# Kernel tuning notes

Hardware: AMD Instinct MI355X
Metric: run time of the kernel (lower is better)

## Reference

```python
import jax, jax.numpy as jnp
import numpy as np

HIDDEN = 512
HEADS = 8
HEAD_DIM = HIDDEN // HEADS


def setup_inputs() -> dict:
    key = jax.random.key(0)
    ks = jax.random.split(key, 7)
    B, C, H, W = 8, HIDDEN, 32, 32
    scale = 1.0 / np.sqrt(C)
    inputs = jax.random.normal(ks[0], (B, C, H, W), dtype=jnp.float32)
    # 1x1 conv == per-pixel linear; store weights as [C_in, C_out]
    wq = jax.random.normal(ks[1], (C, HIDDEN), dtype=jnp.float32) * scale
    wk = jax.random.normal(ks[2], (C, HIDDEN), dtype=jnp.float32) * scale
    wv = jax.random.normal(ks[3], (C, HIDDEN), dtype=jnp.float32) * scale
    bq = jax.random.normal(ks[4], (HIDDEN,), dtype=jnp.float32) * 0.01
    bk = jax.random.normal(ks[5], (HIDDEN,), dtype=jnp.float32) * 0.01
    bv = jax.random.normal(ks[6], (HIDDEN,), dtype=jnp.float32) * 0.01
    return {"inputs": inputs, "wq": wq, "bq": bq, "wk": wk, "bk": bk, "wv": wv, "bv": bv}


def _proj_heads(x, w, b):
    # x: [B,C,H,W] -> tokens [B,heads,N,head_dim], matching transpose_for_scores
    B, C, H, W = x.shape
    t = jnp.einsum('bchw,cd->bhwd', x, w) + b          # [B,H,W,HIDDEN]
    t = t.reshape(B, H * W, HEADS, HEAD_DIM)
    return t.transpose(0, 2, 1, 3)                      # [B,heads,N,hd]


def reference(inputs, wq, bq, wk, bk, wv, bv):
    B, C, H, W = inputs.shape
    q = _proj_heads(inputs, wq, bq)
    k = _proj_heads(inputs, wk, bk)
    v = _proj_heads(inputs, wv, bv)
    # NOTE: original module applies NO 1/sqrt(d) scaling
    scores = jnp.einsum('bhnd,bhmd->bhnm', q, k)        # [B,heads,N,N]
    probs = jax.nn.softmax(scores, axis=-1)
    ctx = jnp.einsum('bhnm,bhmd->bhnd', probs, v)       # [B,heads,N,hd]
    # [B,heads,N,hd] -> [B,N,heads*hd] -> [B,H,W,C] -> [B,C,H,W]
    out = ctx.transpose(0, 2, 1, 3).reshape(B, H, W, HEADS * HEAD_DIM)
    return out.transpose(0, 3, 1, 2)
```

## Files before the change

### kernel.cpp

```cpp
#include <hip/hip_runtime.h>
#include <cmath>

#define B_     8
#define C_     512
#define N_     1024
#define HEADS_ 8
#define HD_    64
#define INST_  64

typedef short v8s  __attribute__((ext_vector_type(8)));
typedef float v16f __attribute__((ext_vector_type(16)));
typedef unsigned short ushort_t;
typedef unsigned int   uint_t;

__device__ inline unsigned short f2bf(float x) {
    unsigned u = __builtin_bit_cast(unsigned, x);
    unsigned r = u + 0x7fffu + ((u >> 16) & 1u);
    return (unsigned short)(r >> 16);
}
__device__ inline float bf2f(unsigned short h) {
    unsigned u = ((unsigned)h) << 16;
    return __builtin_bit_cast(float, u);
}

__global__ __launch_bounds__(256) void prep_kernel(
    const float* __restrict__ x,
    const float* __restrict__ wq, const float* __restrict__ wk,
    const float* __restrict__ wv,
    uint_t* __restrict__ wth, uint_t* __restrict__ wtl,
    uint_t* __restrict__ xth, uint_t* __restrict__ xtl)
{
    __shared__ uint_t LH[64 * 32];
    __shared__ uint_t LL[64 * 32];
    const int z = blockIdx.z;
    const float* src;
    int srcStride;
    size_t outRow0;
    uint_t *oh, *ol;
    if (z < 3) {
        if (blockIdx.x >= 8) return;
        src = (z == 0) ? wq : (z == 1) ? wk : wv;
        srcStride = 512;
        outRow0 = (size_t)z * 512 + blockIdx.x * 64;
        oh = wth; ol = wtl;
    } else {
        int b = z - 3;
        src = x + (size_t)b * C_ * N_;
        srcStride = 1024;
        outRow0 = (size_t)b * 1024 + blockIdx.x * 64;
        oh = xth; ol = xtl;
    }
    const int d0 = blockIdx.x * 64;
    const int c0 = blockIdx.y * 64;
    const int t  = threadIdx.x;

    #pragma unroll
    for (int rep = 0; rep < 2; ++rep) {
        int idx = rep * 256 + t;
        int cp  = idx >> 4;
        int dq  = idx & 15;
        float4 fa = *(const float4*)&src[(size_t)(c0 + 2 * cp) * srcStride + d0 + dq * 4];
        float4 fb = *(const float4*)&src[(size_t)(c0 + 2 * cp + 1) * srcStride + d0 + dq * 4];
        float aa[4] = {fa.x, fa.y, fa.z, fa.w};
        float bb[4] = {fb.x, fb.y, fb.z, fb.w};
        #pragma unroll
        for (int j = 0; j < 4; ++j) {
            int d_l = dq * 4 + j;
            unsigned short ha = f2bf(aa[j]), hb = f2bf(bb[j]);
            unsigned short la = f2bf(aa[j] - bf2f(ha));
            unsigned short lb = f2bf(bb[j] - bf2f(hb));
            LH[d_l * 32 + (cp ^ (d_l & 31))] = (uint_t)ha | ((uint_t)hb << 16);
            LL[d_l * 32 + (cp ^ (d_l & 31))] = (uint_t)la | ((uint_t)lb << 16);
        }
    }
    __syncthreads();

    const int d_l = t >> 2;
    const int wq4 = (t & 3) * 8;
    uint_t vh[8], vl[8];
    #pragma unroll
    for (int i = 0; i < 8; ++i) {
        vh[i] = LH[d_l * 32 + ((wq4 + i) ^ (d_l & 31))];
        vl[i] = LL[d_l * 32 + ((wq4 + i) ^ (d_l & 31))];
    }
    size_t base = (outRow0 + d_l) * 256 + c0 / 2 + wq4;
    *(uint4*)&oh[base]     = *(uint4*)&vh[0];
    *(uint4*)&oh[base + 4] = *(uint4*)&vh[4];
    *(uint4*)&ol[base]     = *(uint4*)&vl[0];
    *(uint4*)&ol[base + 4] = *(uint4*)&vl[4];
}

__global__ __launch_bounds__(256) void proj_kernel(
    const ushort_t* __restrict__ xth, const ushort_t* __restrict__ xtl,
    const ushort_t* __restrict__ wth, const ushort_t* __restrict__ wtl,
    const float* __restrict__ bq, const float* __restrict__ bk,
    const float* __restrict__ bv,
    ushort_t* __restrict__ qh, ushort_t* __restrict__ ql,
    ushort_t* __restrict__ kh, ushort_t* __restrict__ kl,
    ushort_t* __restrict__ vt)
{
    __shared__ uint_t POOL[8192];
    ushort_t* As = (ushort_t*)POOL;
    ushort_t* Bs = (ushort_t*)(POOL + 4096);

    const int tok0  = blockIdx.x * 128;
    const int b     = tok0 >> 10;
    const int ntb   = tok0 & 1023;
    const int by    = blockIdx.y;
    const int which = by >> 2;
    const int nloc0 = (by & 3) * 128;

    const int t   = threadIdx.x;
    const int w   = t >> 6;
    const int l   = t & 63;
    const int l31 = l & 31;
    const int h5  = l >> 5;
    const int wm  = w & 1;
    const int wn  = w >> 1;

    const int g   = t & 7;
    const int r0  = t >> 3;
    const int swz = g ^ (r0 & 7);
    const bool act = (which < 2) || (g < 4);

    const ushort_t* baseA = ((g < 4) ? xth : xtl)
        + (size_t)(tok0 + r0) * 512 + (g & 3) * 8;
    const ushort_t* baseB = ((g < 4) ? wth : wtl)
        + (size_t)(which * 512 + nloc0 + r0) * 512 + (g & 3) * 8;

    v8s pfa[4], pfb[4];

    auto load_tile = [&](int k0) {
        #pragma unroll
        for (int rep = 0; rep < 4; ++rep)
            if (act) {
                pfa[rep] = *(const v8s*)(baseA + rep * 16384 + k0);
                pfb[rep] = *(const v8s*)(baseB + rep * 16384 + k0);
            }
    };
    auto store_tile = [&]() {
        #pragma unroll
        for (int rep = 0; rep < 4; ++rep)
            if (act) {
                int so = ((rep * 32 + r0) * 8 + swz) * 8;
                *(v8s*)&As[so] = pfa[rep];
                *(v8s*)&Bs[so] = pfb[rep];
            }
    };

    v16f acc[2][2] = {{{}, {}}, {{}, {}}};

    load_tile(0);
    store_tile();
    __syncthreads();

    for (int step = 0; step < 16; ++step) {
        if (step < 15) load_tile((step + 1) * 32);

        #pragma unroll
        for (int kc = 0; kc < 2; ++kc) {
            v8s ahf[2], alf[2], bhf[2], blf[2];
            #pragma unroll
            for (int ms = 0; ms < 2; ++ms) {
                int rm = wm * 64 + ms * 32 + l31;
                ahf[ms] = *(v8s*)&As[(rm * 8 + ((kc * 2 + h5) ^ (rm & 7))) * 8];
                if (which < 2)
                    alf[ms] = *(v8s*)&As[(rm * 8 + ((4 + kc * 2 + h5) ^ (rm & 7))) * 8];
            }
            #pragma unroll
            for (int ns = 0; ns < 2; ++ns) {
                int rn = wn * 64 + ns * 32 + l31;
                bhf[ns] = *(v8s*)&Bs[(rn * 8 + ((kc * 2 + h5) ^ (rn & 7))) * 8];
                if (which < 2)
                    blf[ns] = *(v8s*)&Bs[(rn * 8 + ((4 + kc * 2 + h5) ^ (rn & 7))) * 8];
            }
            #pragma unroll
            for (int ms = 0; ms < 2; ++ms)
                #pragma unroll
                for (int ns = 0; ns < 2; ++ns) {
                    acc[ms][ns] = __builtin_amdgcn_mfma_f32_32x32x16_bf16(
                        ahf[ms], bhf[ns], acc[ms][ns], 0, 0, 0);
                    if (which < 2) {
                        acc[ms][ns] = __builtin_amdgcn_mfma_f32_32x32x16_bf16(
                            alf[ms], bhf[ns], acc[ms][ns], 0, 0, 0);
                        acc[ms][ns] = __builtin_amdgcn_mfma_f32_32x32x16_bf16(
                            ahf[ms], blf[ns], acc[ms][ns], 0, 0, 0);
                    }
                }
        }

        __syncthreads();
        if (step < 15) {
            store_tile();
            __syncthreads();
        }
    }

    if (which < 2) {
        ushort_t* oh = (which == 0) ? qh : kh;
        ushort_t* ol = (which == 0) ? ql : kl;
        const float* bias = (which == 0) ? bq : bk;
        #pragma unroll
        for (int ns = 0; ns < 2; ++ns) {
            int d_local = nloc0 + wn * 64 + ns * 32 + l31;
            float bvv  = bias[d_local];
            int head   = d_local >> 6;
            int hd     = d_local & 63;
            size_t pb  = (size_t)(b * HEADS_ + head) * 65536 + hd;
            #pragma unroll
            for (int ms = 0; ms < 2; ++ms)
                #pragma unroll
                for (int r = 0; r < 16; ++r) {
                    int n = ntb + wm * 64 + ms * 32 + (r & 3) + 8 * (r >> 2) + 4 * h5;
                    float val = acc[ms][ns][r] + bvv;
                    unsigned short hbits = f2bf(val);
                    oh[pb + (size_t)n * 64] = hbits;
                    ol[pb + (size_t)n * 64] = f2bf(val - bf2f(hbits));
                }
        }
    } else {
        float bvv[2];
        #pragma unroll
        for (int ns = 0; ns < 2; ++ns)
            bvv[ns] = bv[nloc0 + wn * 64 + ns * 32 + l31];
        __syncthreads();
        uint_t* TW = POOL + w * 2048;
        #pragma unroll
        for (int ms = 0; ms < 2; ++ms)
            #pragma unroll
            for (int ns = 0; ns < 2; ++ns)
                #pragma unroll
                for (int r = 0; r < 16; ++r) {
                    int tok_l = ms * 32 + (r & 3) + 8 * (r >> 2) + 4 * h5;
                    int hd_l  = ns * 32 + l31;
                    unsigned short hbits = f2bf(acc[ms][ns][r] + bvv[ns]);
                    ((ushort_t*)TW)[(hd_l * 32 + ((tok_l >> 1) ^ (hd_l & 31))) * 2
                                    + (tok_l & 1)] = hbits;
                }
        __syncthreads();
        const int head = (nloc0 + wn * 64) >> 6;
        uint_t* vtu = (uint_t*)vt;
        size_t base = (size_t)(b * HEADS_ + head) * 32768 + (size_t)l * 512
                    + (ntb + wm * 64) / 2;
        #pragma unroll
        for (int c = 0; c < 8; ++c) {
            uint_t wd[4];
            #pragma unroll
            for (int kk = 0; kk < 4; ++kk) {
                int ws = c * 4 + kk;
                int w3 = ws & 7;
                int sw = (ws & ~7) | (w3 & 1) | (((w3 >> 1) & 1) << 2)
                                  | (((w3 >> 2) & 1) << 1);
                wd[kk] = TW[l * 32 + (sw ^ (l & 31))];
            }
            *(uint4*)&vtu[base + c * 4] = *(uint4*)&wd[0];
        }
    }
}

__global__ __launch_bounds__(256) void attn_kernel(
    const ushort_t* __restrict__ qh, const ushort_t* __restrict__ ql,
    const ushort_t* __restrict__ kh, const ushort_t* __restrict__ kl,
    const ushort_t* __restrict__ vt, float* __restrict__ out)
{
    __shared__ ushort_t KH[64 * 64];
    __shared__ ushort_t KL[64 * 64];
    __shared__ ushort_t VT[64 * 64];
    __shared__ float    RS[128];

    const int inst  = blockIdx.x;
    const int chunk = blockIdx.y;
    const int t     = threadIdx.x;
    const int w     = t >> 6;
    const int l     = t & 63;
    const int l31   = l & 31;
    const int h5    = l >> 5;

    const ushort_t* Qh = qh + (size_t)inst * 65536;
    const ushort_t* Ql = ql + (size_t)inst * 65536;
    const ushort_t* Kh = kh + (size_t)inst * 65536;
    const ushort_t* Kl = kl + (size_t)inst * 65536;
    const ushort_t* Vt = vt + (size_t)inst * 65536;

    const int qbase = chunk * 128 + w * 32;

    v8s aqh[4], aql[4];
    #pragma unroll
    for (int ks = 0; ks < 4; ++ks) {
        size_t off = (size_t)(qbase + l31) * 64 + ks * 16 + h5 * 8;
        aqh[ks] = *(const v8s*)&Qh[off];
        aql[ks] = *(const v8s*)&Ql[off];
    }

    const int g   = t & 7;
    const int r0  = t >> 3;
    const int swz = g ^ (r0 & 7);
    const ushort_t* baseKh = Kh + (size_t)r0 * 64 + g * 8;
    const ushort_t* baseKl = Kl + (size_t)r0 * 64 + g * 8;
    const ushort_t* baseV  = Vt + (size_t)r0 * 1024 + g * 8;

    v8s pk[2], pl[2], pv[2];
    auto load_tile = [&](int kt) {
        #pragma unroll
        for (int rep = 0; rep < 2; ++rep) {
            pk[rep] = *(const v8s*)(baseKh + (size_t)kt * 4096 + rep * 2048);
            pl[rep] = *(const v8s*)(baseKl + (size_t)kt * 4096 + rep * 2048);
            pv[rep] = *(const v8s*)(baseV + (size_t)rep * 32768 + kt * 64);
        }
    };
    auto store_tile = [&]() {
        #pragma unroll
        for (int rep = 0; rep < 2; ++rep) {
            int so = ((rep * 32 + r0) * 8 + swz) * 8;
            *(v8s*)&KH[so] = pk[rep];
            *(v8s*)&KL[so] = pl[rep];
            *(v8s*)&VT[so] = pv[rep];
        }
    };

    v16f O0 = {}, O1 = {};
    float rsumv = 0.f;

    load_tile(0);
    store_tile();
    __syncthreads();

    for (int kt = 0; kt < 16; ++kt) {
        if (kt < 15) load_tile(kt + 1);

        #pragma unroll
        for (int t2 = 0; t2 < 2; ++t2) {
            v16f s = {};
            int kvrow = t2 * 32 + l31;
            #pragma unroll
            for (int ks = 0; ks < 4; ++ks) {
                int so = (kvrow * 8 + ((ks * 2 + h5) ^ (kvrow & 7))) * 8;
                v8s khf = *(v8s*)&KH[so];
                v8s klf = *(v8s*)&KL[so];
                s = __builtin_amdgcn_mfma_f32_32x32x16_bf16(khf, aqh[ks], s, 0, 0, 0);
                s = __builtin_amdgcn_mfma_f32_32x32x16_bf16(khf, aql[ks], s, 0, 0, 0);
                s = __builtin_amdgcn_mfma_f32_32x32x16_bf16(klf, aqh[ks], s, 0, 0, 0);
            }
            v8s p0, p1;
            #pragma unroll
            for (int j = 0; j < 8; ++j) {
                float e0 = __expf(s[j] - 64.0f);
                float e1 = __expf(s[8 + j] - 64.0f);
                rsumv += e0 + e1;
                p0[j] = (short)f2bf(e0);
                p1[j] = (short)f2bf(e1);
            }
            #pragma unroll
            for (int hh = 0; hh < 2; ++hh) {
                int rv = hh * 32 + l31;
                int g0 = (4 * t2 + h5)     ^ (rv & 7);
                int g1 = (4 * t2 + 2 + h5) ^ (rv & 7);
                v8s bv0 = *(v8s*)&VT[(rv * 8 + g0) * 8];
                v8s bv1 = *(v8s*)&VT[(rv * 8 + g1) * 8];
                if (hh == 0) {
                    O0 = __builtin_amdgcn_mfma_f32_32x32x16_bf16(p0, bv0, O0, 0, 0, 0);
                    O0 = __builtin_amdgcn_mfma_f32_32x32x16_bf16(p1, bv1, O0, 0, 0, 0);
                } else {
                    O1 = __builtin_amdgcn_mfma_f32_32x32x16_bf16(p0, bv0, O1, 0, 0, 0);
                    O1 = __builtin_amdgcn_mfma_f32_32x32x16_bf16(p1, bv1, O1, 0, 0, 0);
                }
            }
        }

        __syncthreads();
        if (kt < 15) {
            store_tile();
            __syncthreads();
        }
    }

    float tot = rsumv + __shfl_xor(rsumv, 32, 64);
    if (h5 == 0) RS[w * 32 + l31] = 1.0f / tot;
    __syncthreads();
    float invr[16];
    #pragma unroll
    for (int r = 0; r < 16; ++r)
        invr[r] = RS[w * 32 + (r & 3) + 8 * (r >> 2) + 4 * h5];

    const int b    = inst >> 3;
    const int head = inst & 7;
    float* ob = out + (size_t)b * C_ * N_;
    #pragma unroll
    for (int hh = 0; hh < 2; ++hh) {
        const v16f& O = hh ? O1 : O0;
        int c = head * 64 + hh * 32 + l31;
        #pragma unroll
        for (int qd = 0; qd < 4; ++qd) {
            int n = qbase + 8 * qd + 4 * h5;
            float4 o4;
            o4.x = O[qd * 4 + 0] * invr[qd * 4 + 0];
            o4.y = O[qd * 4 + 1] * invr[qd * 4 + 1];
            o4.z = O[qd * 4 + 2] * invr[qd * 4 + 2];
            o4.w = O[qd * 4 + 3] * invr[qd * 4 + 3];
            *(float4*)&ob[(size_t)c * N_ + n] = o4;
        }
    }
}

extern "C" void kernel_launch(void* const* d_in, const int* in_sizes, int n_in,
                              void* d_out, int out_size, void* d_ws, size_t ws_size,
                              hipStream_t stream) {
    const float* x  = (const float*)d_in[0];
    const float* wq = (const float*)d_in[1];
    const float* bq = (const float*)d_in[2];
    const float* wk = (const float*)d_in[3];
    const float* bk = (const float*)d_in[4];
    const float* wv = (const float*)d_in[5];
    const float* bv = (const float*)d_in[6];
    float* out = (float*)d_out;

    char* ws = (char*)d_ws;
    ushort_t* wth = (ushort_t*)(ws);
    ushort_t* wtl = (ushort_t*)(ws + 1572864);
    ushort_t* xth = (ushort_t*)(ws + 3145728);
    ushort_t* xtl = (ushort_t*)(ws + 11534336);
    ushort_t* qh  = (ushort_t*)(ws + 19922944);
    ushort_t* ql  = (ushort_t*)(ws + 28311552);
    ushort_t* kh  = (ushort_t*)(ws + 36700160);
    ushort_t* kl  = (ushort_t*)(ws + 45088768);
    ushort_t* vt  = (ushort_t*)(ws + 53477376);

    prep_kernel<<<dim3(16, 8, 11), 256, 0, stream>>>(
        x, wq, wk, wv, (uint_t*)wth, (uint_t*)wtl, (uint_t*)xth, (uint_t*)xtl);
    proj_kernel<<<dim3(64, 12), 256, 0, stream>>>(xth, xtl, wth, wtl,
                                                  bq, bk, bv, qh, ql, kh, kl, vt);
    attn_kernel<<<dim3(64, 8), 256, 0, stream>>>(qh, ql, kh, kl, vt, out);
}
```

Measured before the change: 167.6 us.

## Double-buffer LDS tiles in projection and attention kernels, split prep kernel

Converts the projection and attention main loops to double-buffered shared memory so the next tile is stored into the alternate buffer. This removes one barrier per iteration and issues global loads two steps ahead. It also splits the combined weight and input prep kernel into two kernels, which drops the early-exit blocks. Packed bf16 conversion via the HIP intrinsic replaces scalar conversions in the softmax and V-transpose paths. The cost is doubled LDS use, which may lower occupancy, plus one extra kernel launch.

```diff
diff --git a/kernel.cpp b/kernel.cpp
--- a/kernel.cpp
+++ b/kernel.cpp
@@ -1,4 +1,5 @@
 #include <hip/hip_runtime.h>
+#include <hip/hip_bf16.h>
 #include <cmath>
 
 #define B_     8
@@ -22,34 +23,22 @@
     unsigned u = ((unsigned)h) << 16;
     return __builtin_bit_cast(float, u);
 }
-
-__global__ __launch_bounds__(256) void prep_kernel(
-    const float* __restrict__ x,
+__device__ inline uint_t pkbf(float a, float b) {
+    __hip_bfloat162 p = __float22bfloat162_rn(make_float2(a, b));
+    uint_t r;
+    __builtin_memcpy(&r, &p, 4);
+    return r;
+}
+
+__global__ __launch_bounds__(256) void prep_w_kernel(
     const float* __restrict__ wq, const float* __restrict__ wk,
     const float* __restrict__ wv,
-    uint_t* __restrict__ wth, uint_t* __restrict__ wtl,
-    uint_t* __restrict__ xth, uint_t* __restrict__ xtl)
+    uint_t* __restrict__ wth, uint_t* __restrict__ wtl)
 {
     __shared__ uint_t LH[64 * 32];
     __shared__ uint_t LL[64 * 32];
-    const int z = blockIdx.z;
-    const float* src;
-    int srcStride;
-    size_t outRow0;
-    uint_t *oh, *ol;
-    if (z < 3) {
-        if (blockIdx.x >= 8) return;
-        src = (z == 0) ? wq : (z == 1) ? wk : wv;
-        srcStride = 512;
-        outRow0 = (size_t)z * 512 + blockIdx.x * 64;
-        oh = wth; ol = wtl;
-    } else {
-        int b = z - 3;
-        src = x + (size_t)b * C_ * N_;
-        srcStride = 1024;
-        outRow0 = (size_t)b * 1024 + blockIdx.x * 64;
-        oh = xth; ol = xtl;
-    }
+    const int which = blockIdx.z;
+    const float* __restrict__ src = (which == 0) ? wq : (which == 1) ? wk : wv;
     const int d0 = blockIdx.x * 64;
     const int c0 = blockIdx.y * 64;
     const int t  = threadIdx.x;
@@ -59,8 +48,8 @@
         int idx = rep * 256 + t;
         int cp  = idx >> 4;
         int dq  = idx & 15;
-        float4 fa = *(const float4*)&src[(size_t)(c0 + 2 * cp) * srcStride + d0 + dq * 4];
-        float4 fb = *(const float4*)&src[(size_t)(c0 + 2 * cp + 1) * srcStride + d0 + dq * 4];
+        float4 fa = *(const float4*)&src[(size_t)(c0 + 2 * cp) * 512 + d0 + dq * 4];
+        float4 fb = *(const float4*)&src[(size_t)(c0 + 2 * cp + 1) * 512 + d0 + dq * 4];
         float aa[4] = {fa.x, fa.y, fa.z, fa.w};
         float bb[4] = {fb.x, fb.y, fb.z, fb.w};
         #pragma unroll
@@ -83,11 +72,59 @@
         vh[i] = LH[d_l * 32 + ((wq4 + i) ^ (d_l & 31))];
         vl[i] = LL[d_l * 32 + ((wq4 + i) ^ (d_l & 31))];
     }
-    size_t base = (outRow0 + d_l) * 256 + c0 / 2 + wq4;
-    *(uint4*)&oh[base]     = *(uint4*)&vh[0];
-    *(uint4*)&oh[base + 4] = *(uint4*)&vh[4];
-    *(uint4*)&ol[base]     = *(uint4*)&vl[0];
-    *(uint4*)&ol[base + 4] = *(uint4*)&vl[4];
+    size_t base = ((size_t)which * 512 + d0 + d_l) * 256 + c0 / 2 + wq4;
+    *(uint4*)&wth[base]     = *(uint4*)&vh[0];
+    *(uint4*)&wth[base + 4] = *(uint4*)&vh[4];
+    *(uint4*)&wtl[base]     = *(uint4*)&vl[0];
+    *(uint4*)&wtl[base + 4] = *(uint4*)&vl[4];
+}
+
+__global__ __launch_bounds__(256) void prep_x_kernel(
+    const float* __restrict__ x,
+    uint_t* __restrict__ xth, uint_t* __restrict__ xtl)
+{
+    __shared__ uint_t LH[64 * 32];
+    __shared__ uint_t LL[64 * 32];
+    const int b = blockIdx.z;
+    const float* __restrict__ src = x + (size_t)b * C_ * N_;
+    const int d0 = blockIdx.x * 64;
+    const int c0 = blockIdx.y * 64;
+    const int t  = threadIdx.x;
+
+    #pragma unroll
+    for (int rep = 0; rep < 2; ++rep) {
+        int idx = rep * 256 + t;
+        int cp  = idx >> 4;
+        int dq  = idx & 15;
+        float4 fa = *(const float4*)&src[(size_t)(c0 + 2 * cp) * 1024 + d0 + dq * 4];
+        float4 fb = *(const float4*)&src[(size_t)(c0 + 2 * cp + 1) * 1024 + d0 + dq * 4];
+        float aa[4] = {fa.x, fa.y, fa.z, fa.w};
+        float bb[4] = {fb.x, fb.y, fb.z, fb.w};
+        #pragma unroll
+        for (int j = 0; j < 4; ++j) {
+            int d_l = dq * 4 + j;
+            unsigned short ha = f2bf(aa[j]), hb = f2bf(bb[j]);
+            unsigned short la = f2bf(aa[j] - bf2f(ha));
+            unsigned short lb = f2bf(bb[j] - bf2f(hb));
+            LH[d_l * 32 + (cp ^ (d_l & 31))] = (uint_t)ha | ((uint_t)hb << 16);
+            LL[d_l * 32 + (cp ^ (d_l & 31))] = (uint_t)la | ((uint_t)lb << 16);
+        }
+    }
+    __syncthreads();
+
+    const int d_l = t >> 2;
+    const int wq4 = (t & 3) * 8;
+    uint_t vh[8], vl[8];
+    #pragma unroll
+    for (int i = 0; i < 8; ++i) {
+        vh[i] = LH[d_l * 32 + ((wq4 + i) ^ (d_l & 31))];
+        vl[i] = LL[d_l * 32 + ((wq4 + i) ^ (d_l & 31))];
+    }
+    size_t base = ((size_t)b * 1024 + d0 + d_l) * 256 + c0 / 2 + wq4;
+    *(uint4*)&xth[base]     = *(uint4*)&vh[0];
+    *(uint4*)&xth[base + 4] = *(uint4*)&vh[4];
+    *(uint4*)&xtl[base]     = *(uint4*)&vl[0];
+    *(uint4*)&xtl[base + 4] = *(uint4*)&vl[4];
 }
 
 __global__ __launch_bounds__(256) void proj_kernel(
@@ -99,9 +136,7 @@
     ushort_t* __restrict__ kh, ushort_t* __restrict__ kl,
     ushort_t* __restrict__ vt)
 {
-    __shared__ uint_t POOL[8192];
-    ushort_t* As = (ushort_t*)POOL;
-    ushort_t* Bs = (ushort_t*)(POOL + 4096);
+    __shared__ ushort_t POOL[32768];
 
     const int tok0  = blockIdx.x * 128;
     const int b     = tok0 >> 10;
@@ -138,7 +173,9 @@
                 pfb[rep] = *(const v8s*)(baseB + rep * 16384 + k0);
             }
     };
-    auto store_tile = [&]() {
+    auto store_tile = [&](int buf) {
+        ushort_t* As = POOL + buf * 16384;
+        ushort_t* Bs = As + 8192;
         #pragma unroll
         for (int rep = 0; rep < 4; ++rep)
             if (act) {
@@ -151,11 +188,13 @@
     v16f acc[2][2] = {{{}, {}}, {{}, {}}};
 
     load_tile(0);
-    store_tile();
+    store_tile(0);
+    load_tile(32);
     __syncthreads();
 
     for (int step = 0; step < 16; ++step) {
-        if (step < 15) load_tile((step + 1) * 32);
+        const ushort_t* As = POOL + (step & 1) * 16384;
+        const ushort_t* Bs = As + 8192;
 
         #pragma unroll
         for (int kc = 0; kc < 2; ++kc) {
@@ -163,16 +202,16 @@
             #pragma unroll
             for (int ms = 0; ms < 2; ++ms) {
                 int rm = wm * 64 + ms * 32 + l31;
-                ahf[ms] = *(v8s*)&As[(rm * 8 + ((kc * 2 + h5) ^ (rm & 7))) * 8];
+                ahf[ms] = *(const v8s*)&As[(rm * 8 + ((kc * 2 + h5) ^ (rm & 7))) * 8];
                 if (which < 2)
-                    alf[ms] = *(v8s*)&As[(rm * 8 + ((4 + kc * 2 + h5) ^ (rm & 7))) * 8];
+                    alf[ms] = *(const v8s*)&As[(rm * 8 + ((4 + kc * 2 + h5) ^ (rm & 7))) * 8];
             }
             #pragma unroll
             for (int ns = 0; ns < 2; ++ns) {
                 int rn = wn * 64 + ns * 32 + l31;
-                bhf[ns] = *(v8s*)&Bs[(rn * 8 + ((kc * 2 + h5) ^ (rn & 7))) * 8];
+                bhf[ns] = *(const v8s*)&Bs[(rn * 8 + ((kc * 2 + h5) ^ (rn & 7))) * 8];
                 if (which < 2)
-                    blf[ns] = *(v8s*)&Bs[(rn * 8 + ((4 + kc * 2 + h5) ^ (rn & 7))) * 8];
+                    blf[ns] = *(const v8s*)&Bs[(rn * 8 + ((4 + kc * 2 + h5) ^ (rn & 7))) * 8];
             }
             #pragma unroll
             for (int ms = 0; ms < 2; ++ms)
@@ -189,10 +228,10 @@
                 }
         }
 
-        __syncthreads();
         if (step < 15) {
-            store_tile();
+            store_tile((step + 1) & 1);
             __syncthreads();
+            if (step < 14) load_tile((step + 2) * 32);
         }
     }
 
@@ -224,18 +263,17 @@
         for (int ns = 0; ns < 2; ++ns)
             bvv[ns] = bv[nloc0 + wn * 64 + ns * 32 + l31];
         __syncthreads();
-        uint_t* TW = POOL + w * 2048;
+        uint_t* TW = (uint_t*)POOL + w * 2048;
         #pragma unroll
         for (int ms = 0; ms < 2; ++ms)
             #pragma unroll
             for (int ns = 0; ns < 2; ++ns)
                 #pragma unroll
-                for (int r = 0; r < 16; ++r) {
+                for (int r = 0; r < 16; r += 2) {
                     int tok_l = ms * 32 + (r & 3) + 8 * (r >> 2) + 4 * h5;
                     int hd_l  = ns * 32 + l31;
-                    unsigned short hbits = f2bf(acc[ms][ns][r] + bvv[ns]);
-                    ((ushort_t*)TW)[(hd_l * 32 + ((tok_l >> 1) ^ (hd_l & 31))) * 2
-                                    + (tok_l & 1)] = hbits;
+                    TW[hd_l * 32 + ((tok_l >> 1) ^ (hd_l & 31))] =
+                        pkbf(acc[ms][ns][r] + bvv[ns], acc[ms][ns][r + 1] + bvv[ns]);
                 }
         __syncthreads();
         const int head = (nloc0 + wn * 64) >> 6;
@@ -247,10 +285,10 @@
             uint_t wd[4];
             #pragma unroll
             for (int kk = 0; kk < 4; ++kk) {
-                int ws = c * 4 + kk;
-                int w3 = ws & 7;
-                int sw = (ws & ~7) | (w3 & 1) | (((w3 >> 1) & 1) << 2)
-                                  | (((w3 >> 2) & 1) << 1);
+                int wsx = c * 4 + kk;
+                int w3 = wsx & 7;
+                int sw = (wsx & ~7) | (w3 & 1) | (((w3 >> 1) & 1) << 2)
+                                   | (((w3 >> 2) & 1) << 1);
                 wd[kk] = TW[l * 32 + (sw ^ (l & 31))];
             }
             *(uint4*)&vtu[base + c * 4] = *(uint4*)&wd[0];
@@ -263,9 +301,7 @@
     const ushort_t* __restrict__ kh, const ushort_t* __restrict__ kl,
     const ushort_t* __restrict__ vt, float* __restrict__ out)
 {
-    __shared__ ushort_t KH[64 * 64];
-    __shared__ ushort_t KL[64 * 64];
-    __shared__ ushort_t VT[64 * 64];
+    __shared__ ushort_t POOL[24576];
     __shared__ float    RS[128];
 
     const int inst  = blockIdx.x;
@@ -308,7 +344,10 @@
             pv[rep] = *(const v8s*)(baseV + (size_t)rep * 32768 + kt * 64);
         }
     };
-    auto store_tile = [&]() {
+    auto store_tile = [&](int buf) {
+        ushort_t* KH = POOL + buf * 12288;
+        ushort_t* KL = KH + 4096;
+        ushort_t* VT = KL + 4096;
         #pragma unroll
         for (int rep = 0; rep < 2; ++rep) {
             int so = ((rep * 32 + r0) * 8 + swz) * 8;
@@ -322,11 +361,14 @@
     float rsumv = 0.f;
 
     load_tile(0);
-    store_tile();
+    store_tile(0);
+    load_tile(1);
     __syncthreads();
 
     for (int kt = 0; kt < 16; ++kt) {
-        if (kt < 15) load_tile(kt + 1);
+        const ushort_t* KH = POOL + (kt & 1) * 12288;
+        const ushort_t* KL = KH + 4096;
+        const ushort_t* VT = KL + 4096;
 
         #pragma unroll
         for (int t2 = 0; t2 < 2; ++t2) {
@@ -335,28 +377,34 @@
             #pragma unroll
             for (int ks = 0; ks < 4; ++ks) {
                 int so = (kvrow * 8 + ((ks * 2 + h5) ^ (kvrow & 7))) * 8;
-                v8s khf = *(v8s*)&KH[so];
-                v8s klf = *(v8s*)&KL[so];
+                v8s khf = *(const v8s*)&KH[so];
+                v8s klf = *(const v8s*)&KL[so];
                 s = __builtin_amdgcn_mfma_f32_32x32x16_bf16(khf, aqh[ks], s, 0, 0, 0);
                 s = __builtin_amdgcn_mfma_f32_32x32x16_bf16(khf, aql[ks], s, 0, 0, 0);
                 s = __builtin_amdgcn_mfma_f32_32x32x16_bf16(klf, aqh[ks], s, 0, 0, 0);
             }
-            v8s p0, p1;
+            float e0[8], e1[8];
             #pragma unroll
             for (int j = 0; j < 8; ++j) {
-                float e0 = __expf(s[j] - 64.0f);
-                float e1 = __expf(s[8 + j] - 64.0f);
-                rsumv += e0 + e1;
-                p0[j] = (short)f2bf(e0);
-                p1[j] = (short)f2bf(e1);
-            }
+                e0[j] = __expf(s[j] - 64.0f);
+                e1[j] = __expf(s[8 + j] - 64.0f);
+                rsumv += e0[j] + e1[j];
+            }
+            uint4 u0, u1;
+            u0.x = pkbf(e0[0], e0[1]); u0.y = pkbf(e0[2], e0[3]);
+            u0.z = pkbf(e0[4], e0[5]); u0.w = pkbf(e0[6], e0[7]);
+            u1.x = pkbf(e1[0], e1[1]); u1.y = pkbf(e1[2], e1[3]);
+            u1.z = pkbf(e1[4], e1[5]); u1.w = pkbf(e1[6], e1[7]);
+            v8s p0 = __builtin_bit_cast(v8s, u0);
+            v8s p1 = __builtin_bit_cast(v8s, u1);
+
             #pragma unroll
             for (int hh = 0; hh < 2; ++hh) {
                 int rv = hh * 32 + l31;
                 int g0 = (4 * t2 + h5)     ^ (rv & 7);
                 int g1 = (4 * t2 + 2 + h5) ^ (rv & 7);
-                v8s bv0 = *(v8s*)&VT[(rv * 8 + g0) * 8];
-                v8s bv1 = *(v8s*)&VT[(rv * 8 + g1) * 8];
+                v8s bv0 = *(const v8s*)&VT[(rv * 8 + g0) * 8];
+                v8s bv1 = *(const v8s*)&VT[(rv * 8 + g1) * 8];
                 if (hh == 0) {
                     O0 = __builtin_amdgcn_mfma_f32_32x32x16_bf16(p0, bv0, O0, 0, 0, 0);
                     O0 = __builtin_amdgcn_mfma_f32_32x32x16_bf16(p1, bv1, O0, 0, 0, 0);
@@ -367,10 +415,10 @@
             }
         }
 
-        __syncthreads();
         if (kt < 15) {
-            store_tile();
+            store_tile((kt + 1) & 1);
             __syncthreads();
+            if (kt < 14) load_tile(kt + 2);
         }
     }
 
@@ -425,8 +473,9 @@
     ushort_t* kl  = (ushort_t*)(ws + 45088768);
     ushort_t* vt  = (ushort_t*)(ws + 53477376);
 
-    prep_kernel<<<dim3(16, 8, 11), 256, 0, stream>>>(
-        x, wq, wk, wv, (uint_t*)wth, (uint_t*)wtl, (uint_t*)xth, (uint_t*)xtl);
+    prep_w_kernel<<<dim3(8, 8, 3), 256, 0, stream>>>(wq, wk, wv,
+                                                     (uint_t*)wth, (uint_t*)wtl);
+    prep_x_kernel<<<dim3(16, 8, 8), 256, 0, stream>>>(x, (uint_t*)xth, (uint_t*)xtl);
     proj_kernel<<<dim3(64, 12), 256, 0, stream>>>(xth, xtl, wth, wtl,
                                                   bq, bk, bv, qh, ql, kh, kl, vt);
     attn_kernel<<<dim3(64, 8), 256, 0, stream>>>(qh, ql, kh, kl, vt, out);
```

After: 179.1 us. 1.07x slower.

## Replace split-bf16 emulation with single fp16 MFMA for projections and QK scores

Applied to the files above, without the earlier changes.

Drops the hi/lo bf16 split (three MFMAs per product) in both the projection GEMM and the QK^T score computation and uses a single fp16 MFMA instead. x, W, Q and K are stored as fp16, which halves workspace traffic and LDS footprint and removes two thirds of the MFMAs in those stages. Softmax probabilities and V are now packed to bf16 with a paired conversion intrinsic. This trades accuracy for speed: the unscaled scores are sensitive to reduced mantissa, and fp16 range could overflow for large values.

```diff
diff --git a/kernel.cpp b/kernel.cpp
--- a/kernel.cpp
+++ b/kernel.cpp
@@ -1,4 +1,5 @@
 #include <hip/hip_runtime.h>
+#include <hip/hip_bf16.h>
 #include <cmath>
 
 #define B_     8
@@ -8,47 +9,45 @@
 #define HD_    64
 #define INST_  64
 
-typedef short v8s  __attribute__((ext_vector_type(8)));
-typedef float v16f __attribute__((ext_vector_type(16)));
+typedef short     v8s __attribute__((ext_vector_type(8)));
+typedef _Float16  v8h __attribute__((ext_vector_type(8)));
+typedef float    v16f __attribute__((ext_vector_type(16)));
 typedef unsigned short ushort_t;
 typedef unsigned int   uint_t;
 
-__device__ inline unsigned short f2bf(float x) {
-    unsigned u = __builtin_bit_cast(unsigned, x);
-    unsigned r = u + 0x7fffu + ((u >> 16) & 1u);
-    return (unsigned short)(r >> 16);
-}
-__device__ inline float bf2f(unsigned short h) {
-    unsigned u = ((unsigned)h) << 16;
-    return __builtin_bit_cast(float, u);
+__device__ inline ushort_t f2h(float x) {
+    _Float16 h = (_Float16)x;
+    ushort_t r; __builtin_memcpy(&r, &h, 2); return r;
+}
+__device__ inline uint_t pkbf(float a, float b) {
+    __hip_bfloat162 p = __float22bfloat162_rn(make_float2(a, b));
+    uint_t r; __builtin_memcpy(&r, &p, 4); return r;
 }
 
 __global__ __launch_bounds__(256) void prep_kernel(
     const float* __restrict__ x,
     const float* __restrict__ wq, const float* __restrict__ wk,
     const float* __restrict__ wv,
-    uint_t* __restrict__ wth, uint_t* __restrict__ wtl,
-    uint_t* __restrict__ xth, uint_t* __restrict__ xtl)
+    uint_t* __restrict__ wt, uint_t* __restrict__ xt)
 {
     __shared__ uint_t LH[64 * 32];
-    __shared__ uint_t LL[64 * 32];
     const int z = blockIdx.z;
     const float* src;
     int srcStride;
     size_t outRow0;
-    uint_t *oh, *ol;
+    uint_t* oh;
     if (z < 3) {
         if (blockIdx.x >= 8) return;
         src = (z == 0) ? wq : (z == 1) ? wk : wv;
         srcStride = 512;
         outRow0 = (size_t)z * 512 + blockIdx.x * 64;
-        oh = wth; ol = wtl;
+        oh = wt;
     } else {
         int b = z - 3;
         src = x + (size_t)b * C_ * N_;
         srcStride = 1024;
         outRow0 = (size_t)b * 1024 + blockIdx.x * 64;
-        oh = xth; ol = xtl;
+        oh = xt;
     }
     const int d0 = blockIdx.x * 64;
     const int c0 = blockIdx.y * 64;
@@ -66,42 +65,33 @@
         #pragma unroll
         for (int j = 0; j < 4; ++j) {
             int d_l = dq * 4 + j;
-            unsigned short ha = f2bf(aa[j]), hb = f2bf(bb[j]);
-            unsigned short la = f2bf(aa[j] - bf2f(ha));
-            unsigned short lb = f2bf(bb[j] - bf2f(hb));
-            LH[d_l * 32 + (cp ^ (d_l & 31))] = (uint_t)ha | ((uint_t)hb << 16);
-            LL[d_l * 32 + (cp ^ (d_l & 31))] = (uint_t)la | ((uint_t)lb << 16);
+            LH[d_l * 32 + (cp ^ (d_l & 31))] =
+                (uint_t)f2h(aa[j]) | ((uint_t)f2h(bb[j]) << 16);
         }
     }
     __syncthreads();
 
     const int d_l = t >> 2;
     const int wq4 = (t & 3) * 8;
-    uint_t vh[8], vl[8];
-    #pragma unroll
-    for (int i = 0; i < 8; ++i) {
+    uint_t vh[8];
+    #pragma unroll
+    for (int i = 0; i < 8; ++i)
         vh[i] = LH[d_l * 32 + ((wq4 + i) ^ (d_l & 31))];
-        vl[i] = LL[d_l * 32 + ((wq4 + i) ^ (d_l & 31))];
-    }
     size_t base = (outRow0 + d_l) * 256 + c0 / 2 + wq4;
     *(uint4*)&oh[base]     = *(uint4*)&vh[0];
     *(uint4*)&oh[base + 4] = *(uint4*)&vh[4];
-    *(uint4*)&ol[base]     = *(uint4*)&vl[0];
-    *(uint4*)&ol[base + 4] = *(uint4*)&vl[4];
 }
 
 __global__ __launch_bounds__(256) void proj_kernel(
-    const ushort_t* __restrict__ xth, const ushort_t* __restrict__ xtl,
-    const ushort_t* __restrict__ wth, const ushort_t* __restrict__ wtl,
+    const _Float16* __restrict__ xt, const _Float16* __restrict__ wt,
     const float* __restrict__ bq, const float* __restrict__ bk,
     const float* __restrict__ bv,
-    ushort_t* __restrict__ qh, ushort_t* __restrict__ ql,
-    ushort_t* __restrict__ kh, ushort_t* __restrict__ kl,
+    ushort_t* __restrict__ qf, ushort_t* __restrict__ kf,
     ushort_t* __restrict__ vt)
 {
-    __shared__ uint_t POOL[8192];
-    ushort_t* As = (ushort_t*)POOL;
-    ushort_t* Bs = (ushort_t*)(POOL + 4096);
+    __shared__ _Float16 POOL[16384];
+    _Float16* As = POOL;
+    _Float16* Bs = POOL + 4096;
 
     const int tok0  = blockIdx.x * 128;
     const int b     = tok0 >> 10;
@@ -118,34 +108,28 @@
     const int wm  = w & 1;
     const int wn  = w >> 1;
 
-    const int g   = t & 7;
-    const int r0  = t >> 3;
-    const int swz = g ^ (r0 & 7);
-    const bool act = (which < 2) || (g < 4);
-
-    const ushort_t* baseA = ((g < 4) ? xth : xtl)
-        + (size_t)(tok0 + r0) * 512 + (g & 3) * 8;
-    const ushort_t* baseB = ((g < 4) ? wth : wtl)
-        + (size_t)(which * 512 + nloc0 + r0) * 512 + (g & 3) * 8;
-
-    v8s pfa[4], pfb[4];
-
+    const int g   = t & 3;
+    const int r0  = t >> 2;
+    const int swz = g ^ (r0 & 3);
+
+    const _Float16* baseA = xt + (size_t)(tok0 + r0) * 512 + g * 8;
+    const _Float16* baseB = wt + (size_t)(which * 512 + nloc0 + r0) * 512 + g * 8;
+
+    v8h pfa[2], pfb[2];
     auto load_tile = [&](int k0) {
         #pragma unroll
-        for (int rep = 0; rep < 4; ++rep)
-            if (act) {
-                pfa[rep] = *(const v8s*)(baseA + rep * 16384 + k0);
-                pfb[rep] = *(const v8s*)(baseB + rep * 16384 + k0);
-            }
+        for (int rep = 0; rep < 2; ++rep) {
+            pfa[rep] = *(const v8h*)(baseA + rep * 32768 + k0);
+            pfb[rep] = *(const v8h*)(baseB + rep * 32768 + k0);
+        }
     };
     auto store_tile = [&]() {
         #pragma unroll
-        for (int rep = 0; rep < 4; ++rep)
-            if (act) {
-                int so = ((rep * 32 + r0) * 8 + swz) * 8;
-                *(v8s*)&As[so] = pfa[rep];
-                *(v8s*)&Bs[so] = pfb[rep];
-            }
+        for (int rep = 0; rep < 2; ++rep) {
+            int so = ((rep * 64 + r0) * 4 + swz) * 8;
+            *(v8h*)&As[so] = pfa[rep];
+            *(v8h*)&Bs[so] = pfb[rep];
+        }
     };
 
     v16f acc[2][2] = {{{}, {}}, {{}, {}}};
@@ -159,34 +143,23 @@
 
         #pragma unroll
         for (int kc = 0; kc < 2; ++kc) {
-            v8s ahf[2], alf[2], bhf[2], blf[2];
+            v8h af[2], bf[2];
             #pragma unroll
             for (int ms = 0; ms < 2; ++ms) {
                 int rm = wm * 64 + ms * 32 + l31;
-                ahf[ms] = *(v8s*)&As[(rm * 8 + ((kc * 2 + h5) ^ (rm & 7))) * 8];
-                if (which < 2)
-                    alf[ms] = *(v8s*)&As[(rm * 8 + ((4 + kc * 2 + h5) ^ (rm & 7))) * 8];
+                af[ms] = *(const v8h*)&As[(rm * 4 + ((kc * 2 + h5) ^ (rm & 3))) * 8];
             }
             #pragma unroll
             for (int ns = 0; ns < 2; ++ns) {
                 int rn = wn * 64 + ns * 32 + l31;
-                bhf[ns] = *(v8s*)&Bs[(rn * 8 + ((kc * 2 + h5) ^ (rn & 7))) * 8];
-                if (which < 2)
-                    blf[ns] = *(v8s*)&Bs[(rn * 8 + ((4 + kc * 2 + h5) ^ (rn & 7))) * 8];
+                bf[ns] = *(const v8h*)&Bs[(rn * 4 + ((kc * 2 + h5) ^ (rn & 3))) * 8];
             }
             #pragma unroll
             for (int ms = 0; ms < 2; ++ms)
                 #pragma unroll
-                for (int ns = 0; ns < 2; ++ns) {
-                    acc[ms][ns] = __builtin_amdgcn_mfma_f32_32x32x16_bf16(
-                        ahf[ms], bhf[ns], acc[ms][ns], 0, 0, 0);
-                    if (which < 2) {
-                        acc[ms][ns] = __builtin_amdgcn_mfma_f32_32x32x16_bf16(
-                            alf[ms], bhf[ns], acc[ms][ns], 0, 0, 0);
-                        acc[ms][ns] = __builtin_amdgcn_mfma_f32_32x32x16_bf16(
-                            ahf[ms], blf[ns], acc[ms][ns], 0, 0, 0);
-                    }
-                }
+                for (int ns = 0; ns < 2; ++ns)
+                    acc[ms][ns] = __builtin_amdgcn_mfma_f32_32x32x16_f16(
+                        af[ms], bf[ns], acc[ms][ns], 0, 0, 0);
         }
 
         __syncthreads();
@@ -197,8 +170,7 @@
     }
 
     if (which < 2) {
-        ushort_t* oh = (which == 0) ? qh : kh;
-        ushort_t* ol = (which == 0) ? ql : kl;
+        ushort_t* oh = (which == 0) ? qf : kf;
         const float* bias = (which == 0) ? bq : bk;
         #pragma unroll
         for (int ns = 0; ns < 2; ++ns) {
@@ -212,10 +184,7 @@
                 #pragma unroll
                 for (int r = 0; r < 16; ++r) {
                     int n = ntb + wm * 64 + ms * 32 + (r & 3) + 8 * (r >> 2) + 4 * h5;
-                    float val = acc[ms][ns][r] + bvv;
-                    unsigned short hbits = f2bf(val);
-                    oh[pb + (size_t)n * 64] = hbits;
-                    ol[pb + (size_t)n * 64] = f2bf(val - bf2f(hbits));
+                    oh[pb + (size_t)n * 64] = f2h(acc[ms][ns][r] + bvv);
                 }
         }
     } else {
@@ -224,18 +193,17 @@
         for (int ns = 0; ns < 2; ++ns)
             bvv[ns] = bv[nloc0 + wn * 64 + ns * 32 + l31];
         __syncthreads();
-        uint_t* TW = POOL + w * 2048;
+        uint_t* TW = (uint_t*)POOL + w * 2048;
         #pragma unroll
         for (int ms = 0; ms < 2; ++ms)
             #pragma unroll
             for (int ns = 0; ns < 2; ++ns)
                 #pragma unroll
-                for (int r = 0; r < 16; ++r) {
+                for (int r = 0; r < 16; r += 2) {
                     int tok_l = ms * 32 + (r & 3) + 8 * (r >> 2) + 4 * h5;
                     int hd_l  = ns * 32 + l31;
-                    unsigned short hbits = f2bf(acc[ms][ns][r] + bvv[ns]);
-                    ((ushort_t*)TW)[(hd_l * 32 + ((tok_l >> 1) ^ (hd_l & 31))) * 2
-                                    + (tok_l & 1)] = hbits;
+                    TW[hd_l * 32 + ((tok_l >> 1) ^ (hd_l & 31))] =
+                        pkbf(acc[ms][ns][r] + bvv[ns], acc[ms][ns][r + 1] + bvv[ns]);
                 }
         __syncthreads();
         const int head = (nloc0 + wn * 64) >> 6;
@@ -247,10 +215,10 @@
             uint_t wd[4];
             #pragma unroll
             for (int kk = 0; kk < 4; ++kk) {
-                int ws = c * 4 + kk;
-                int w3 = ws & 7;
-                int sw = (ws & ~7) | (w3 & 1) | (((w3 >> 1) & 1) << 2)
-                                  | (((w3 >> 2) & 1) << 1);
+                int wsx = c * 4 + kk;
+                int w3 = wsx & 7;
+                int sw = (wsx & ~7) | (w3 & 1) | (((w3 >> 1) & 1) << 2)
+                                   | (((w3 >> 2) & 1) << 1);
                 wd[kk] = TW[l * 32 + (sw ^ (l & 31))];
             }
             *(uint4*)&vtu[base + c * 4] = *(uint4*)&wd[0];
@@ -259,13 +227,11 @@
 }
 
 __global__ __launch_bounds__(256) void attn_kernel(
-    const ushort_t* __restrict__ qh, const ushort_t* __restrict__ ql,
-    const ushort_t* __restrict__ kh, const ushort_t* __restrict__ kl,
+    const ushort_t* __restrict__ qf, const ushort_t* __restrict__ kf,
     const ushort_t* __restrict__ vt, float* __restrict__ out)
 {
-    __shared__ ushort_t KH[64 * 64];
-    __shared__ ushort_t KL[64 * 64];
-    __shared__ ushort_t VT[64 * 64];
+    __shared__ _Float16 KH[4096];
+    __shared__ ushort_t VT[4096];
     __shared__ float    RS[128];
 
     const int inst  = blockIdx.x;
@@ -276,35 +242,28 @@
     const int l31   = l & 31;
     const int h5    = l >> 5;
 
-    const ushort_t* Qh = qh + (size_t)inst * 65536;
-    const ushort_t* Ql = ql + (size_t)inst * 65536;
-    const ushort_t* Kh = kh + (size_t)inst * 65536;
-    const ushort_t* Kl = kl + (size_t)inst * 65536;
+    const ushort_t* Qf = qf + (size_t)inst * 65536;
+    const ushort_t* Kf = kf + (size_t)inst * 65536;
     const ushort_t* Vt = vt + (size_t)inst * 65536;
 
     const int qbase = chunk * 128 + w * 32;
 
-    v8s aqh[4], aql[4];
-    #pragma unroll
-    for (int ks = 0; ks < 4; ++ks) {
-        size_t off = (size_t)(qbase + l31) * 64 + ks * 16 + h5 * 8;
-        aqh[ks] = *(const v8s*)&Qh[off];
-        aql[ks] = *(const v8s*)&Ql[off];
-    }
+    v8h aq[4];
+    #pragma unroll
+    for (int ks = 0; ks < 4; ++ks)
+        aq[ks] = *(const v8h*)&Qf[(size_t)(qbase + l31) * 64 + ks * 16 + h5 * 8];
 
     const int g   = t & 7;
     const int r0  = t >> 3;
     const int swz = g ^ (r0 & 7);
-    const ushort_t* baseKh = Kh + (size_t)r0 * 64 + g * 8;
-    const ushort_t* baseKl = Kl + (size_t)r0 * 64 + g * 8;
-    const ushort_t* baseV  = Vt + (size_t)r0 * 1024 + g * 8;
-
-    v8s pk[2], pl[2], pv[2];
+    const ushort_t* baseK = Kf + (size_t)r0 * 64 + g * 8;
+    const ushort_t* baseV = Vt + (size_t)r0 * 1024 + g * 8;
+
+    v8h pk[2]; v8s pv[2];
     auto load_tile = [&](int kt) {
         #pragma unroll
         for (int rep = 0; rep < 2; ++rep) {
-            pk[rep] = *(const v8s*)(baseKh + (size_t)kt * 4096 + rep * 2048);
-            pl[rep] = *(const v8s*)(baseKl + (size_t)kt * 4096 + rep * 2048);
+            pk[rep] = *(const v8h*)(baseK + (size_t)kt * 4096 + rep * 2048);
             pv[rep] = *(const v8s*)(baseV + (size_t)rep * 32768 + kt * 64);
         }
     };
@@ -312,8 +271,7 @@
         #pragma unroll
         for (int rep = 0; rep < 2; ++rep) {
             int so = ((rep * 32 + r0) * 8 + swz) * 8;
-            *(v8s*)&KH[so] = pk[rep];
-            *(v8s*)&KL[so] = pl[rep];
+            *(v8h*)&KH[so] = pk[rep];
             *(v8s*)&VT[so] = pv[rep];
         }
     };
@@ -335,28 +293,31 @@
             #pragma unroll
             for (int ks = 0; ks < 4; ++ks) {
                 int so = (kvrow * 8 + ((ks * 2 + h5) ^ (kvrow & 7))) * 8;
-                v8s khf = *(v8s*)&KH[so];
-                v8s klf = *(v8s*)&KL[so];
-                s = __builtin_amdgcn_mfma_f32_32x32x16_bf16(khf, aqh[ks], s, 0, 0, 0);
-                s = __builtin_amdgcn_mfma_f32_32x32x16_bf16(khf, aql[ks], s, 0, 0, 0);
-                s = __builtin_amdgcn_mfma_f32_32x32x16_bf16(klf, aqh[ks], s, 0, 0, 0);
-            }
-            v8s p0, p1;
+                v8h khf = *(const v8h*)&KH[so];
+                s = __builtin_amdgcn_mfma_f32_32x32x16_f16(khf, aq[ks], s, 0, 0, 0);
+            }
+            float e0[8], e1[8];
             #pragma unroll
             for (int j = 0; j < 8; ++j) {
-                float e0 = __expf(s[j] - 64.0f);
-                float e1 = __expf(s[8 + j] - 64.0f);
-                rsumv += e0 + e1;
-                p0[j] = (short)f2bf(e0);
-                p1[j] = (short)f2bf(e1);
-            }
+                e0[j] = __expf(s[j] - 64.0f);
+                e1[j] = __expf(s[8 + j] - 64.0f);
+                rsumv += e0[j] + e1[j];
+            }
+            uint4 u0, u1;
+            u0.x = pkbf(e0[0], e0[1]); u0.y = pkbf(e0[2], e0[3]);
+            u0.z = pkbf(e0[4], e0[5]); u0.w = pkbf(e0[6], e0[7]);
+            u1.x = pkbf(e1[0], e1[1]); u1.y = pkbf(e1[2], e1[3]);
+            u1.z = pkbf(e1[4], e1[5]); u1.w = pkbf(e1[6], e1[7]);
+            v8s p0 = __builtin_bit_cast(v8s, u0);
+            v8s p1 = __builtin_bit_cast(v8s, u1);
+
             #pragma unroll
             for (int hh = 0; hh < 2; ++hh) {
                 int rv = hh * 32 + l31;
                 int g0 = (4 * t2 + h5)     ^ (rv & 7);
                 int g1 = (4 * t2 + 2 + h5) ^ (rv & 7);
-                v8s bv0 = *(v8s*)&VT[(rv * 8 + g0) * 8];
-                v8s bv1 = *(v8s*)&VT[(rv * 8 + g1) * 8];
+                v8s bv0 = *(const v8s*)&VT[(rv * 8 + g0) * 8];
+                v8s bv1 = *(const v8s*)&VT[(rv * 8 + g1) * 8];
                 if (hh == 0) {
                     O0 = __builtin_amdgcn_mfma_f32_32x32x16_bf16(p0, bv0, O0, 0, 0, 0);
                     O0 = __builtin_amdgcn_mfma_f32_32x32x16_bf16(p1, bv1, O0, 0, 0, 0);
@@ -415,19 +376,15 @@
     float* out = (float*)d_out;
 
     char* ws = (char*)d_ws;
-    ushort_t* wth = (ushort_t*)(ws);
-    ushort_t* wtl = (ushort_t*)(ws + 1572864);
-    ushort_t* xth = (ushort_t*)(ws + 3145728);
-    ushort_t* xtl = (ushort_t*)(ws + 11534336);
-    ushort_t* qh  = (ushort_t*)(ws + 19922944);
-    ushort_t* ql  = (ushort_t*)(ws + 28311552);
-    ushort_t* kh  = (ushort_t*)(ws + 36700160);
-    ushort_t* kl  = (ushort_t*)(ws + 45088768);
-    ushort_t* vt  = (ushort_t*)(ws + 53477376);
+    _Float16* wt = (_Float16*)(ws);
+    _Float16* xt = (_Float16*)(ws + 1572864);
+    ushort_t* qf = (ushort_t*)(ws + 9961472);
+    ushort_t* kf = (ushort_t*)(ws + 18350080);
+    ushort_t* vt = (ushort_t*)(ws + 26738688);
 
     prep_kernel<<<dim3(16, 8, 11), 256, 0, stream>>>(
-        x, wq, wk, wv, (uint_t*)wth, (uint_t*)wtl, (uint_t*)xth, (uint_t*)xtl);
-    proj_kernel<<<dim3(64, 12), 256, 0, stream>>>(xth, xtl, wth, wtl,
-                                                  bq, bk, bv, qh, ql, kh, kl, vt);
-    attn_kernel<<<dim3(64, 8), 256, 0, stream>>>(qh, ql, kh, kl, vt, out);
-}
+        x, wq, wk, wv, (uint_t*)wt, (uint_t*)xt);
+    proj_kernel<<<dim3(64, 12), 256, 0, stream>>>(xt, wt, bq, bk, bv,
+                                                  qf, kf, vt);
+    attn_kernel<<<dim3(64, 8), 256, 0, stream>>>(qf, kf, vt, out);
+}
```

Result: faster. 140.8 us (-16.0%).
